# Kernel tuning notes

Hardware: AMD Instinct MI355X
Metric: run time of the kernel (lower is better)

The kernel has to match this reference:

```python
import jax, jax.numpy as jnp
import numpy as np

C = 64          # channels / d_model
D_INNER = 128   # expand * C
D_STATE = 16
D_CONV = 4
DT_RANK = 4     # ceil(C / 16)
GROUPS = 4
EPS = 1e-5


def setup_inputs() -> dict:
    key = jax.random.key(0)
    ks = jax.random.split(key, 12)
    b, h, w = 2, 128, 128
    s = 0.02
    return {
        "x": jax.random.normal(ks[0], (b, C, h, w), jnp.float32),
        "in_proj_w": jax.random.normal(ks[1], (2 * D_INNER, C), jnp.float32) * s,
        "conv_w": jax.random.normal(ks[2], (D_INNER, D_CONV), jnp.float32) * s,
        "conv_b": jnp.zeros((D_INNER,), jnp.float32),
        "x_proj_w": jax.random.normal(ks[3], (DT_RANK + 2 * D_STATE, D_INNER), jnp.float32) * s,
        "dt_proj_w": jax.random.normal(ks[4], (D_INNER, DT_RANK), jnp.float32) * s,
        "dt_proj_b": jax.random.normal(ks[5], (D_INNER,), jnp.float32) * s,
        "A_log": jnp.log(jnp.broadcast_to(jnp.arange(1, D_STATE + 1, dtype=jnp.float32), (D_INNER, D_STATE))),
        "D": jnp.ones((D_INNER,), jnp.float32),
        "out_proj_w": jax.random.normal(ks[6], (C, D_INNER), jnp.float32) * s,
        "gn_scale": jnp.ones((C,), jnp.float32),
        "gn_bias": jnp.zeros((C,), jnp.float32),
    }


def _mamba(xr, in_proj_w, conv_w, conv_b, x_proj_w, dt_proj_w, dt_proj_b, A_log, D, out_proj_w):
    # xr: (b, L, C)
    b, L, _ = xr.shape
    xz = jnp.einsum('blc,ec->ble', xr, in_proj_w)          # (b, L, 2*d_inner)
    xc, z = jnp.split(xz, 2, axis=-1)
    # causal depthwise conv1d, kernel D_CONV
    xp = jnp.pad(xc, ((0, 0), (D_CONV - 1, 0), (0, 0)))
    xconv = sum(conv_w[:, k] * xp[:, k:k + L, :] for k in range(D_CONV)) + conv_b
    u = jax.nn.silu(xconv)                                  # (b, L, d_inner)
    dbc = jnp.einsum('bld,ed->ble', u, x_proj_w)
    dt_r = dbc[..., :DT_RANK]
    Bm = dbc[..., DT_RANK:DT_RANK + D_STATE]                # (b, L, d_state)
    Cm = dbc[..., DT_RANK + D_STATE:]                       # (b, L, d_state)
    dt = jax.nn.softplus(jnp.einsum('blr,dr->bld', dt_r, dt_proj_w) + dt_proj_b)
    A = -jnp.exp(A_log)                                     # (d_inner, d_state)
    deltaA = jnp.exp(dt[..., None] * A)                     # (b, L, d_inner, d_state)
    deltaBu = (dt * u)[..., None] * Bm[:, :, None, :]       # (b, L, d_inner, d_state)

    def step(hst, inp):
        dA_t, dBu_t, C_t = inp
        hst = dA_t * hst + dBu_t                            # (b, d_inner, d_state)
        y_t = jnp.einsum('bds,bs->bd', hst, C_t)
        return hst, y_t

    h0 = jnp.zeros((b, D_INNER, D_STATE), xr.dtype)
    _, ys = jax.lax.scan(step, h0, (jnp.moveaxis(deltaA, 1, 0), jnp.moveaxis(deltaBu, 1, 0), jnp.moveaxis(Cm, 1, 0)))
    y = jnp.moveaxis(ys, 0, 1) + u * D                      # (b, L, d_inner)
    y = y * jax.nn.silu(z)
    return jnp.einsum('bld,cd->blc', y, out_proj_w)


def _group_norm_silu(x, scale, bias):
    # x: (b, C, h, w)
    b, c, h, w = x.shape
    xg = x.reshape(b, GROUPS, c // GROUPS, h, w)
    mu = xg.mean(axis=(2, 3, 4), keepdims=True)
    var = xg.var(axis=(2, 3, 4), keepdims=True)
    xn = ((xg - mu) * jax.lax.rsqrt(var + EPS)).reshape(b, c, h, w)
    return jax.nn.silu(xn * scale[None, :, None, None] + bias[None, :, None, None])


def reference(x, in_proj_w, conv_w, conv_b, x_proj_w, dt_proj_w, dt_proj_b, A_log, D, out_proj_w, gn_scale, gn_bias):
    b, c, h, w = x.shape
    xr = jnp.transpose(x, (0, 2, 3, 1)).reshape(b, h * w, c)
    y = _mamba(xr, in_proj_w, conv_w, conv_b, x_proj_w, dt_proj_w, dt_proj_b, A_log, D, out_proj_w)
    y = jnp.transpose(y.reshape(b, h, w, c), (0, 3, 1, 2))
    y = _group_norm_silu(y, gn_scale, gn_bias)
    return y + x
```

## Files before the change

### kernel.cpp

```cpp
#include <hip/hip_runtime.h>

#define BB 2
#define CCH 64
#define LLEN 16384
#define DM 128
#define NCHK 512
#define TCHK 32
#define NGRP 32
#define JG 16
#define NG 4

#define OFF_XC   0ull
#define OFF_HEND 0ull
#define OFF_HLOC 2097152ull
#define OFF_Z    4194304ull
#define OFF_U    8388608ull
#define OFF_DT   12582912ull
#define OFF_BM   16777216ull
#define OFF_CM   17301504ull
#define OFF_DTS  17825792ull
#define OFF_YM   17956864ull
#define OFF_WC   17956864ull
#define OFF_STAT 20054016ull
#define OFF_CUMDT 20971520ull
#define OFF_GEND  21102592ull
#define OFF_GDT   21233664ull
#define OFF_GINIT 21241856ull

__device__ __forceinline__ float fsilu(float v) {
  return v * __builtin_amdgcn_rcpf(1.f + __expf(-v));
}
__device__ __forceinline__ float fsoftplus(float v) {
  return v > 20.f ? v : __logf(1.f + __expf(v));
}
__device__ __forceinline__ unsigned short f2bf(float f) {
  unsigned u = __builtin_bit_cast(unsigned, f);
  u += 0x7fffu + ((u >> 16) & 1u);
  return (unsigned short)(u >> 16);
}
__device__ __forceinline__ float bf2f(unsigned short h) {
  unsigned u = (unsigned)h << 16;
  return __builtin_bit_cast(float, u);
}

__global__ __launch_bounds__(256) void k0_wcomb(
    const float* __restrict__ xpw, const float* __restrict__ dtw, float* __restrict__ wc,
    float* __restrict__ stat)
{
  int i = blockIdx.x * 256 + threadIdx.x;
  if (blockIdx.x == 0 && threadIdx.x < BB * NG * 2) stat[threadIdx.x] = 0.f;
  if (i >= 160 * 128) return;
  int e = i >> 7, dd = i & 127;
  float v;
  if (e < 128) {
    v = dtw[e * 4 + 0] * xpw[0 * 128 + dd] + dtw[e * 4 + 1] * xpw[1 * 128 + dd]
      + dtw[e * 4 + 2] * xpw[2 * 128 + dd] + dtw[e * 4 + 3] * xpw[3 * 128 + dd];
  } else {
    v = xpw[(e - 128 + 4) * 128 + dd];
  }
  wc[i] = v;
}

__global__ __launch_bounds__(256) void k1_inproj(
    const float* __restrict__ x, const float* __restrict__ w,
    float* __restrict__ xc, float* __restrict__ z)
{
  const int b = blockIdx.z;
  const int l0 = blockIdx.x * 64;
  const int e0 = blockIdx.y * 64;
  __shared__ float As[64][68];
  __shared__ float Bs[64][68];
  const int t = threadIdx.x;
#pragma unroll
  for (int i = 0; i < 4; i++) {
    int f4 = t + i * 256;
    int c = f4 >> 4, tok4 = (f4 & 15) * 4;
    *reinterpret_cast<float4*>(&As[c][tok4]) =
        *reinterpret_cast<const float4*>(&x[(size_t)(b * CCH + c) * LLEN + l0 + tok4]);
  }
#pragma unroll
  for (int i = 0; i < 16; i++) {
    int idx = t + i * 256;
    int e = idx >> 6, c = idx & 63;
    Bs[c][e] = w[(e0 + e) * CCH + c];
  }
  __syncthreads();
  const int tm = (t & 15) * 4;
  const int tn = (t >> 4) * 4;
  float acc[4][4] = {};
  for (int c = 0; c < 64; c++) {
    float4 av = *reinterpret_cast<const float4*>(&As[c][tm]);
    float4 bv = *reinterpret_cast<const float4*>(&Bs[c][tn]);
    acc[0][0] += av.x * bv.x; acc[0][1] += av.x * bv.y; acc[0][2] += av.x * bv.z; acc[0][3] += av.x * bv.w;
    acc[1][0] += av.y * bv.x; acc[1][1] += av.y * bv.y; acc[1][2] += av.y * bv.z; acc[1][3] += av.y * bv.w;
    acc[2][0] += av.z * bv.x; acc[2][1] += av.z * bv.y; acc[2][2] += av.z * bv.z; acc[2][3] += av.z * bv.w;
    acc[3][0] += av.w * bv.x; acc[3][1] += av.w * bv.y; acc[3][2] += av.w * bv.z; acc[3][3] += av.w * bv.w;
  }
  float* dst = (e0 < DM) ? (xc + e0) : (z + (e0 - DM));
#pragma unroll
  for (int i = 0; i < 4; i++) {
    int l = l0 + tm + i;
    float4 v = make_float4(acc[i][0], acc[i][1], acc[i][2], acc[i][3]);
    *reinterpret_cast<float4*>(dst + (size_t)(b * LLEN + l) * DM + tn) = v;
  }
}

__global__ __launch_bounds__(256) void k2a_conv(
    const float* __restrict__ xc, const float* __restrict__ cw, const float* __restrict__ cb,
    float* __restrict__ u)
{
  const int t = threadIdx.x;
  const int d4 = (t & 31) * 4;
  const int tg = t >> 5;
  const int tok0 = blockIdx.x * 64 + tg * 8;
  const int l0 = tok0 & (LLEN - 1);
  float4 w0 = *reinterpret_cast<const float4*>(cw + (d4 + 0) * 4);
  float4 w1 = *reinterpret_cast<const float4*>(cw + (d4 + 1) * 4);
  float4 w2 = *reinterpret_cast<const float4*>(cw + (d4 + 2) * 4);
  float4 w3 = *reinterpret_cast<const float4*>(cw + (d4 + 3) * 4);
  float4 bias = *reinterpret_cast<const float4*>(cb + d4);
  float4 row[11];
#pragma unroll
  for (int r = 0; r < 11; r++) {
    int l = l0 - 3 + r;
    if (l < 0) row[r] = make_float4(0.f, 0.f, 0.f, 0.f);
    else row[r] = *reinterpret_cast<const float4*>(xc + (size_t)(tok0 - 3 + r) * DM + d4);
  }
#pragma unroll
  for (int j = 0; j < 8; j++) {
    float4 acc;
    acc.x = bias.x + w0.x * row[j].x + w0.y * row[j+1].x + w0.z * row[j+2].x + w0.w * row[j+3].x;
    acc.y = bias.y + w1.x * row[j].y + w1.y * row[j+1].y + w1.z * row[j+2].y + w1.w * row[j+3].y;
    acc.z = bias.z + w2.x * row[j].z + w2.y * row[j+1].z + w2.z * row[j+2].z + w2.w * row[j+3].z;
    acc.w = bias.w + w3.x * row[j].w + w3.y * row[j+1].w + w3.z * row[j+2].w + w3.w * row[j+3].w;
    acc.x = fsilu(acc.x); acc.y = fsilu(acc.y); acc.z = fsilu(acc.z); acc.w = fsilu(acc.w);
    *reinterpret_cast<float4*>(u + (size_t)(tok0 + j) * DM + d4) = acc;
  }
}

__global__ __launch_bounds__(128) void k2b_proj(
    const float* __restrict__ u, const float* __restrict__ wc, const float* __restrict__ dtpb,
    float* __restrict__ dt, float* __restrict__ bm, float* __restrict__ cm)
{
  const int tok0 = blockIdx.x * 64;
  const int e0 = blockIdx.y * 32;
  const int t = threadIdx.x;
  __shared__ float As[64][68];
  __shared__ float Bs[64][36];
  const int tm = (t & 15) * 4;
  const int tn = (t >> 4) * 4;
  float acc[4][4] = {};
  for (int kb = 0; kb < 2; kb++) {
#pragma unroll
    for (int i2 = 0; i2 < 2; i2++) {
      int tile = t + i2 * 128;
      int kt4 = (tile & 15) * 4, tok4 = (tile >> 4) * 4;
      const float* gp = u + (size_t)(tok0 + tok4) * DM + kb * 64 + kt4;
      float4 r0 = *reinterpret_cast<const float4*>(gp + 0 * DM);
      float4 r1 = *reinterpret_cast<const float4*>(gp + 1 * DM);
      float4 r2 = *reinterpret_cast<const float4*>(gp + 2 * DM);
      float4 r3 = *reinterpret_cast<const float4*>(gp + 3 * DM);
      *reinterpret_cast<float4*>(&As[kt4 + 0][tok4]) = make_float4(r0.x, r1.x, r2.x, r3.x);
      *reinterpret_cast<float4*>(&As[kt4 + 1][tok4]) = make_float4(r0.y, r1.y, r2.y, r3.y);
      *reinterpret_cast<float4*>(&As[kt4 + 2][tok4]) = make_float4(r0.z, r1.z, r2.z, r3.z);
      *reinterpret_cast<float4*>(&As[kt4 + 3][tok4]) = make_float4(r0.w, r1.w, r2.w, r3.w);
    }
    {
      int kt4 = (t & 15) * 4, et4 = (t >> 4) * 4;
      const float* gp = wc + (size_t)(e0 + et4) * DM + kb * 64 + kt4;
      float4 r0 = *reinterpret_cast<const float4*>(gp + 0 * DM);
      float4 r1 = *reinterpret_cast<const float4*>(gp + 1 * DM);
      float4 r2 = *reinterpret_cast<const float4*>(gp + 2 * DM);
      float4 r3 = *reinterpret_cast<const float4*>(gp + 3 * DM);
      *reinterpret_cast<float4*>(&Bs[kt4 + 0][et4]) = make_float4(r0.x, r1.x, r2.x, r3.x);
      *reinterpret_cast<float4*>(&Bs[kt4 + 1][et4]) = make_float4(r0.y, r1.y, r2.y, r3.y);
      *reinterpret_cast<float4*>(&Bs[kt4 + 2][et4]) = make_float4(r0.z, r1.z, r2.z, r3.z);
      *reinterpret_cast<float4*>(&Bs[kt4 + 3][et4]) = make_float4(r0.w, r1.w, r2.w, r3.w);
    }
    __syncthreads();
#pragma unroll 4
    for (int k = 0; k < 64; k++) {
      float4 av = *reinterpret_cast<const float4*>(&As[k][tm]);
      float4 bv = *reinterpret_cast<const float4*>(&Bs[k][tn]);
      acc[0][0] += av.x * bv.x; acc[0][1] += av.x * bv.y; acc[0][2] += av.x * bv.z; acc[0][3] += av.x * bv.w;
      acc[1][0] += av.y * bv.x; acc[1][1] += av.y * bv.y; acc[1][2] += av.y * bv.z; acc[1][3] += av.y * bv.w;
      acc[2][0] += av.z * bv.x; acc[2][1] += av.z * bv.y; acc[2][2] += av.z * bv.z; acc[2][3] += av.z * bv.w;
      acc[3][0] += av.w * bv.x; acc[3][1] += av.w * bv.y; acc[3][2] += av.w * bv.z; acc[3][3] += av.w * bv.w;
    }
    __syncthreads();
  }
  float* Cs = &As[0][0];
#pragma unroll
  for (int i = 0; i < 4; i++) {
#pragma unroll
    for (int j = 0; j < 4; j++) Cs[(tm + i) * 33 + tn + j] = acc[i][j];
  }
  __syncthreads();
  if (e0 < DM) {
#pragma unroll
    for (int i = 0; i < 16; i++) {
      int idx = t + i * 128;
      int tok = idx >> 5, e = idx & 31;
      float v = fsoftplus(Cs[tok * 33 + e] + dtpb[e0 + e]);
      dt[(size_t)(tok0 + tok) * DM + e0 + e] = v;
    }
  } else {
#pragma unroll
    for (int i = 0; i < 16; i++) {
      int idx = t + i * 128;
      int tok = idx >> 5, e = idx & 31;
      float v = Cs[tok * 33 + e];
      if (e < 16) bm[(size_t)(tok0 + tok) * 16 + e] = v;
      else        cm[(size_t)(tok0 + tok) * 16 + (e - 16)] = v;
    }
  }
}

__global__ __launch_bounds__(128) void k3_scan1(
    const float* __restrict__ dt, const float* __restrict__ u, const float* __restrict__ bm,
    const float* __restrict__ alog, float* __restrict__ hend, float* __restrict__ dts)
{
  const int b = blockIdx.y, ch = blockIdx.x;
  const int d = threadIdx.x;
  __shared__ float sb[TCHK][16];
  const size_t tok0 = (size_t)b * LLEN + (size_t)ch * TCHK;
  reinterpret_cast<float4*>(&sb[0][0])[d] = reinterpret_cast<const float4*>(bm + tok0 * 16)[d];
  float A[16];
  {
    const float4* ap = reinterpret_cast<const float4*>(alog + d * 16);
#pragma unroll
    for (int q = 0; q < 4; q++) {
      float4 v = ap[q];
      A[q * 4 + 0] = -__expf(v.x); A[q * 4 + 1] = -__expf(v.y);
      A[q * 4 + 2] = -__expf(v.z); A[q * 4 + 3] = -__expf(v.w);
    }
  }
  __syncthreads();
  float h[16];
#pragma unroll
  for (int s = 0; s < 16; s++) h[s] = 0.f;
  float dsum = 0.f;
  const float* dtp = dt + tok0 * DM + d;
  const float* up  = u  + tok0 * DM + d;
  for (int i = 0; i < TCHK; i++) {
    float dtv = dtp[(size_t)i * DM];
    float uv  = up[(size_t)i * DM];
    float dtu = dtv * uv;
    dsum += dtv;
    float bv[16];
#pragma unroll
    for (int q = 0; q < 4; q++)
      *reinterpret_cast<float4*>(&bv[q * 4]) = *reinterpret_cast<const float4*>(&sb[i][q * 4]);
#pragma unroll
    for (int s = 0; s < 16; s++) {
      float da = __expf(dtv * A[s]);
      h[s] = da * h[s] + dtu * bv[s];
    }
  }
  float* hp = hend + ((size_t)(b * DM + d) * NCHK + ch) * 16;
#pragma unroll
  for (int q = 0; q < 4; q++)
    reinterpret_cast<float4*>(hp)[q] = make_float4(h[q*4], h[q*4+1], h[q*4+2], h[q*4+3]);
  dts[(size_t)(b * DM + d) * NCHK + ch] = dsum;
}

__global__ __launch_bounds__(256) void k4a_group(
    const float* __restrict__ alog, const float* __restrict__ dts, const float* __restrict__ hend,
    float* __restrict__ hlocal, float* __restrict__ cumdt,
    float* __restrict__ gend, float* __restrict__ gdt)
{
  const int tid = blockIdx.x * 256 + threadIdx.x;
  const int s = tid & 15;
  const int bdg = tid >> 4;
  const int g = bdg & (NGRP - 1);
  const int bd = bdg >> 5;
  const int d = bd & (DM - 1);
  const float A = -__expf(alog[d * 16 + s]);
  const int ch0 = g * JG;
  const float* hp = hend + ((size_t)bd * NCHK + ch0) * 16 + s;
  const float* dp = dts + (size_t)bd * NCHK + ch0;
  float* hl = hlocal + ((size_t)bd * NCHK + ch0) * 16 + s;
  float hb[JG], db[JG];
#pragma unroll
  for (int j = 0; j < JG; j++) { hb[j] = hp[j * 16]; db[j] = dp[j]; }
  float h = 0.f, cd = 0.f;
#pragma unroll
  for (int j = 0; j < JG; j++) {
    hl[j * 16] = h;
    if (s == 0) cumdt[(size_t)(ch0 + j) * (BB * DM) + bd] = cd;
    h = __expf(A * db[j]) * h + hb[j];
    cd += db[j];
  }
  gend[(size_t)bdg * 16 + s] = h;
  if (s == 0) gdt[bdg] = cd;
}

__global__ __launch_bounds__(64) void k4b_combine(
    const float* __restrict__ alog, const float* __restrict__ gdt, const float* __restrict__ gend,
    float* __restrict__ ginit)
{
  const int tid = blockIdx.x * 64 + threadIdx.x;
  const int s = tid & 15, bd = tid >> 4, d = bd & (DM - 1);
  const float A = -__expf(alog[d * 16 + s]);
  const float* ge = gend + (size_t)bd * NGRP * 16 + s;
  const float* gd = gdt + (size_t)bd * NGRP;
  float* gi = ginit + (size_t)bd * NGRP * 16 + s;
  float gb[NGRP], db[NGRP];
#pragma unroll
  for (int g = 0; g < NGRP; g++) { gb[g] = ge[g * 16]; db[g] = gd[g]; }
  float h = 0.f;
#pragma unroll
  for (int g = 0; g < NGRP; g++) {
    gi[g * 16] = h;
    h = __expf(A * db[g]) * h + gb[g];
  }
}

__global__ __launch_bounds__(256) void k5f_scan_out(
    const float* __restrict__ dt, const float* __restrict__ u, const float* __restrict__ bm,
    const float* __restrict__ cm, const float* __restrict__ alog, const float* __restrict__ Dv,
    const float* __restrict__ z, const float* __restrict__ hlocal,
    const float* __restrict__ cumdt, const float* __restrict__ ginit,
    const float* __restrict__ ow, float* __restrict__ ym, float* __restrict__ stat)
{
  const int b = blockIdx.y, bx = blockIdx.x;
  const int t = threadIdx.x;
  const int ch2 = t >> 7;
  const int d = t & 127;
  const int ch = bx * 2 + ch2;
  __shared__ float sb[2][TCHK][16];
  __shared__ float sc[2][TCHK][16];
  __shared__ unsigned short Ysb[DM][72];
  __shared__ unsigned short Bsb[DM][68];
  const size_t tokb = (size_t)b * LLEN + (size_t)bx * 64;
  const size_t tok0 = tokb + (size_t)ch2 * TCHK;
  reinterpret_cast<float4*>(&sb[0][0][0])[t] = reinterpret_cast<const float4*>(bm + tokb * 16)[t];
  reinterpret_cast<float4*>(&sc[0][0][0])[t] = reinterpret_cast<const float4*>(cm + tokb * 16)[t];
#pragma unroll
  for (int i2 = 0; i2 < 2; i2++) {
    int tile = t + i2 * 256;
    int c4 = (tile & 15) * 4;
    int dl4 = (tile >> 4) * 4;
    const float* gp = ow + (size_t)c4 * DM + dl4;
    float4 r0 = *reinterpret_cast<const float4*>(gp + 0 * DM);
    float4 r1 = *reinterpret_cast<const float4*>(gp + 1 * DM);
    float4 r2 = *reinterpret_cast<const float4*>(gp + 2 * DM);
    float4 r3 = *reinterpret_cast<const float4*>(gp + 3 * DM);
    ushort4 w0 = make_ushort4(f2bf(r0.x), f2bf(r1.x), f2bf(r2.x), f2bf(r3.x));
    ushort4 w1 = make_ushort4(f2bf(r0.y), f2bf(r1.y), f2bf(r2.y), f2bf(r3.y));
    ushort4 w2 = make_ushort4(f2bf(r0.z), f2bf(r1.z), f2bf(r2.z), f2bf(r3.z));
    ushort4 w3 = make_ushort4(f2bf(r0.w), f2bf(r1.w), f2bf(r2.w), f2bf(r3.w));
    *reinterpret_cast<ushort4*>(&Bsb[dl4 + 0][c4]) = w0;
    *reinterpret_cast<ushort4*>(&Bsb[dl4 + 1][c4]) = w1;
    *reinterpret_cast<ushort4*>(&Bsb[dl4 + 2][c4]) = w2;
    *reinterpret_cast<ushort4*>(&Bsb[dl4 + 3][c4]) = w3;
  }
  float A[16];
  {
    const float4* ap = reinterpret_cast<const float4*>(alog + d * 16);
#pragma unroll
    for (int q = 0; q < 4; q++) {
      float4 v = ap[q];
      A[q * 4 + 0] = -__expf(v.x); A[q * 4 + 1] = -__expf(v.y);
      A[q * 4 + 2] = -__expf(v.z); A[q * 4 + 3] = -__expf(v.w);
    }
  }
  const float Dd = Dv[d];
  const int bd = b * DM + d;
  const int g = ch / JG;
  const float cd = cumdt[(size_t)ch * (BB * DM) + bd];
  float h[16];
  {
    const float4* hlp = reinterpret_cast<const float4*>(hlocal + ((size_t)bd * NCHK + ch) * 16);
    const float4* gip = reinterpret_cast<const float4*>(ginit + ((size_t)(bd * NGRP + g)) * 16);
#pragma unroll
    for (int q = 0; q < 4; q++) {
      float4 hl = hlp[q];
      float4 gi = gip[q];
      h[q * 4 + 0] = __expf(A[q * 4 + 0] * cd) * gi.x + hl.x;
      h[q * 4 + 1] = __expf(A[q * 4 + 1] * cd) * gi.y + hl.y;
      h[q * 4 + 2] = __expf(A[q * 4 + 2] * cd) * gi.z + hl.z;
      h[q * 4 + 3] = __expf(A[q * 4 + 3] * cd) * gi.w + hl.w;
    }
  }
  __syncthreads();
  const float* dtp = dt + tok0 * DM + d;
  const float* up = u + tok0 * DM + d;
  const float* zp = z + tok0 * DM + d;
  for (int i = 0; i < TCHK; i++) {
    float dtv = dtp[(size_t)i * DM];
    float uv  = up[(size_t)i * DM];
    float zv  = zp[(size_t)i * DM];
    float dtu = dtv * uv;
    float bv[16], cv[16];
#pragma unroll
    for (int q = 0; q < 4; q++) {
      *reinterpret_cast<float4*>(&bv[q * 4]) = *reinterpret_cast<const float4*>(&sb[ch2][i][q * 4]);
      *reinterpret_cast<float4*>(&cv[q * 4]) = *reinterpret_cast<const float4*>(&sc[ch2][i][q * 4]);
    }
    float y = 0.f;
#pragma unroll
    for (int s = 0; s < 16; s++) {
      float da = __expf(dtv * A[s]);
      h[s] = da * h[s] + dtu * bv[s];
      y += h[s] * cv[s];
    }
    Ysb[d][ch2 * TCHK + i] = f2bf((y + uv * Dd) * fsilu(zv));
  }
  __syncthreads();
  const int tm = (t & 15) * 4;
  const int tn = (t >> 4) * 4;
  float acc[4][4] = {};
  for (int k = 0; k < DM; k++) {
    ushort4 a4 = *reinterpret_cast<const ushort4*>(&Ysb[k][tm]);
    ushort4 b4 = *reinterpret_cast<const ushort4*>(&Bsb[k][tn]);
    float ax = bf2f(a4.x), ay = bf2f(a4.y), az = bf2f(a4.z), aw = bf2f(a4.w);
    float bx2 = bf2f(b4.x), by = bf2f(b4.y), bz = bf2f(b4.z), bw = bf2f(b4.w);
    acc[0][0] += ax * bx2; acc[0][1] += ax * by; acc[0][2] += ax * bz; acc[0][3] += ax * bw;
    acc[1][0] += ay * bx2; acc[1][1] += ay * by; acc[1][2] += ay * bz; acc[1][3] += ay * bw;
    acc[2][0] += az * bx2; acc[2][1] += az * by; acc[2][2] += az * bz; acc[2][3] += az * bw;
    acc[3][0] += aw * bx2; acc[3][1] += aw * by; acc[3][2] += aw * bz; acc[3][3] += aw * bw;
  }
  float lsum = 0.f, lssq = 0.f;
#pragma unroll
  for (int i = 0; i < 4; i++) {
    float4 v = make_float4(acc[i][0], acc[i][1], acc[i][2], acc[i][3]);
    *reinterpret_cast<float4*>(ym + (tokb + tm + i) * 64 + tn) = v;
    lsum += v.x + v.y + v.z + v.w;
    lssq += v.x * v.x + v.y * v.y + v.z * v.z + v.w * v.w;
  }
  __shared__ float sg[NG * 2];
  if (t < NG * 2) sg[t] = 0.f;
  __syncthreads();
  const int gg = tn >> 4;
  atomicAdd(&sg[gg * 2 + 0], lsum);
  atomicAdd(&sg[gg * 2 + 1], lssq);
  __syncthreads();
  if (t < NG * 2) atomicAdd(&stat[b * NG * 2 + t], sg[t]);
}

__global__ __launch_bounds__(256) void k7_gn(
    const float* __restrict__ ym, const float* __restrict__ stat,
    const float* __restrict__ scale, const float* __restrict__ bias,
    const float* __restrict__ x, float* __restrict__ out)
{
  const int b = blockIdx.y;
  const int p0 = blockIdx.x * 64;
  const int t = threadIdx.x;
  __shared__ float Ts[64][65];
#pragma unroll
  for (int i = 0; i < 16; i++) {
    int idx = t + i * 256;
    int p = idx >> 6, c = idx & 63;
    Ts[c][p] = ym[(size_t)(b * LLEN + p0 + p) * 64 + c];
  }
  __syncthreads();
  const float invN = 1.f / (16.f * 16384.f);
#pragma unroll
  for (int i = 0; i < 16; i++) {
    int idx = t + i * 256;
    int c = idx >> 6, p = idx & 63;
    int g = c >> 4;
    float mu = stat[b * 8 + g * 2] * invN;
    float var = stat[b * 8 + g * 2 + 1] * invN - mu * mu;
    float rs = rsqrtf(var + 1e-5f);
    float v = (Ts[c][p] - mu) * rs * scale[c] + bias[c];
    size_t o = (size_t)(b * CCH + c) * LLEN + p0 + p;
    out[o] = fsilu(v) + x[o];
  }
}

extern "C" void kernel_launch(void* const* d_in, const int* in_sizes, int n_in,
                              void* d_out, int out_size, void* d_ws, size_t ws_size,
                              hipStream_t stream)
{
  const float* x    = (const float*)d_in[0];
  const float* ipw  = (const float*)d_in[1];
  const float* cw   = (const float*)d_in[2];
  const float* cb   = (const float*)d_in[3];
  const float* xpw  = (const float*)d_in[4];
  const float* dtw  = (const float*)d_in[5];
  const float* dtpb = (const float*)d_in[6];
  const float* alog = (const float*)d_in[7];
  const float* Dv   = (const float*)d_in[8];
  const float* ow   = (const float*)d_in[9];
  const float* gns  = (const float*)d_in[10];
  const float* gnb  = (const float*)d_in[11];

  float* ws    = (float*)d_ws;
  float* xc    = ws + OFF_XC;
  float* hend  = ws + OFF_HEND;
  float* hloc  = ws + OFF_HLOC;
  float* z     = ws + OFF_Z;
  float* u     = ws + OFF_U;
  float* dt    = ws + OFF_DT;
  float* bm    = ws + OFF_BM;
  float* cm    = ws + OFF_CM;
  float* dts   = ws + OFF_DTS;
  float* ym    = ws + OFF_YM;
  float* wc    = ws + OFF_WC;
  float* cumdt = ws + OFF_CUMDT;
  float* gend  = ws + OFF_GEND;
  float* gdt   = ws + OFF_GDT;
  float* ginit = ws + OFF_GINIT;
  float* stat  = ws + OFF_STAT;
  float* out   = (float*)d_out;

  k0_wcomb<<<dim3(80), 256, 0, stream>>>(xpw, dtw, wc, stat);
  k1_inproj<<<dim3(LLEN / 64, 4, BB), 256, 0, stream>>>(x, ipw, xc, z);
  k2a_conv<<<dim3(BB * LLEN / 64), 256, 0, stream>>>(xc, cw, cb, u);
  k2b_proj<<<dim3(BB * LLEN / 64, 5), 128, 0, stream>>>(u, wc, dtpb, dt, bm, cm);
  k3_scan1<<<dim3(NCHK, BB), 128, 0, stream>>>(dt, u, bm, alog, hend, dts);
  k4a_group<<<dim3(BB * DM * NGRP * 16 / 256), 256, 0, stream>>>(alog, dts, hend, hloc, cumdt, gend, gdt);
  k4b_combine<<<dim3(BB * DM * 16 / 64), 64, 0, stream>>>(alog, gdt, gend, ginit);
  k5f_scan_out<<<dim3(NCHK / 2, BB), 256, 0, stream>>>(dt, u, bm, cm, alog, Dv, z, hloc, cumdt, ginit, ow, ym, stat);
  k7_gn<<<dim3(LLEN / 64, BB), 256, 0, stream>>>(ym, stat, gns, gnb, x, out);
}
```

Measured before the change: 136.1 us.

## Halve scan chunk length to double parallel chunks and use 512-thread scan-out blocks

After: 141.8 us. 1.04x slower.

```diff
diff --git a/kernel.cpp b/kernel.cpp
--- a/kernel.cpp
+++ b/kernel.cpp
@@ -4,28 +4,28 @@
 #define CCH 64
 #define LLEN 16384
 #define DM 128
-#define NCHK 512
-#define TCHK 32
+#define NCHK 1024
+#define TCHK 16
 #define NGRP 32
-#define JG 16
+#define JG 32
 #define NG 4
 
-#define OFF_XC   0ull
-#define OFF_HEND 0ull
-#define OFF_HLOC 2097152ull
-#define OFF_Z    4194304ull
-#define OFF_U    8388608ull
-#define OFF_DT   12582912ull
-#define OFF_BM   16777216ull
-#define OFF_CM   17301504ull
-#define OFF_DTS  17825792ull
-#define OFF_YM   17956864ull
-#define OFF_WC   17956864ull
-#define OFF_STAT 20054016ull
-#define OFF_CUMDT 20971520ull
-#define OFF_GEND  21102592ull
-#define OFF_GDT   21233664ull
-#define OFF_GINIT 21241856ull
+#define OFF_XC    0ull
+#define OFF_HEND  0ull
+#define OFF_Z     4194304ull
+#define OFF_U     8388608ull
+#define OFF_DT    12582912ull
+#define OFF_BM    16777216ull
+#define OFF_CM    17301504ull
+#define OFF_DTS   17825792ull
+#define OFF_YM    18088192ull
+#define OFF_WC    18088192ull
+#define OFF_STAT  20185344ull
+#define OFF_HLOC  20185600ull
+#define OFF_CUMDT 24379904ull
+#define OFF_GEND  24642048ull
+#define OFF_GDT   24773120ull
+#define OFF_GINIT 24781312ull
 
 __device__ __forceinline__ float fsilu(float v) {
   return v * __builtin_amdgcn_rcpf(1.f + __expf(-v));
@@ -224,7 +224,8 @@
   const int d = threadIdx.x;
   __shared__ float sb[TCHK][16];
   const size_t tok0 = (size_t)b * LLEN + (size_t)ch * TCHK;
-  reinterpret_cast<float4*>(&sb[0][0])[d] = reinterpret_cast<const float4*>(bm + tok0 * 16)[d];
+  if (d < TCHK * 4)
+    reinterpret_cast<float4*>(&sb[0][0])[d] = reinterpret_cast<const float4*>(bm + tok0 * 16)[d];
   float A[16];
   {
     const float4* ap = reinterpret_cast<const float4*>(alog + d * 16);
@@ -316,7 +317,7 @@
   }
 }
 
-__global__ __launch_bounds__(256) void k5f_scan_out(
+__global__ __launch_bounds__(512) void k5f_scan_out(
     const float* __restrict__ dt, const float* __restrict__ u, const float* __restrict__ bm,
     const float* __restrict__ cm, const float* __restrict__ alog, const float* __restrict__ Dv,
     const float* __restrict__ z, const float* __restrict__ hlocal,
@@ -325,22 +326,22 @@
 {
   const int b = blockIdx.y, bx = blockIdx.x;
   const int t = threadIdx.x;
-  const int ch2 = t >> 7;
+  const int ch4 = t >> 7;
   const int d = t & 127;
-  const int ch = bx * 2 + ch2;
-  __shared__ float sb[2][TCHK][16];
-  __shared__ float sc[2][TCHK][16];
+  const int ch = bx * 4 + ch4;
+  __shared__ float sb[4][TCHK][16];
+  __shared__ float sc[4][TCHK][16];
   __shared__ unsigned short Ysb[DM][72];
   __shared__ unsigned short Bsb[DM][68];
   const size_t tokb = (size_t)b * LLEN + (size_t)bx * 64;
-  const size_t tok0 = tokb + (size_t)ch2 * TCHK;
-  reinterpret_cast<float4*>(&sb[0][0][0])[t] = reinterpret_cast<const float4*>(bm + tokb * 16)[t];
-  reinterpret_cast<float4*>(&sc[0][0][0])[t] = reinterpret_cast<const float4*>(cm + tokb * 16)[t];
-#pragma unroll
-  for (int i2 = 0; i2 < 2; i2++) {
-    int tile = t + i2 * 256;
-    int c4 = (tile & 15) * 4;
-    int dl4 = (tile >> 4) * 4;
+  const size_t tok0 = tokb + (size_t)ch4 * TCHK;
+  if (t < 256) {
+    reinterpret_cast<float4*>(&sb[0][0][0])[t] = reinterpret_cast<const float4*>(bm + tokb * 16)[t];
+    reinterpret_cast<float4*>(&sc[0][0][0])[t] = reinterpret_cast<const float4*>(cm + tokb * 16)[t];
+  }
+  {
+    int c4 = (t & 15) * 4;
+    int dl4 = (t >> 4) * 4;
     const float* gp = ow + (size_t)c4 * DM + dl4;
     float4 r0 = *reinterpret_cast<const float4*>(gp + 0 * DM);
     float4 r1 = *reinterpret_cast<const float4*>(gp + 1 * DM);
@@ -395,8 +396,8 @@
     float bv[16], cv[16];
 #pragma unroll
     for (int q = 0; q < 4; q++) {
-      *reinterpret_cast<float4*>(&bv[q * 4]) = *reinterpret_cast<const float4*>(&sb[ch2][i][q * 4]);
-      *reinterpret_cast<float4*>(&cv[q * 4]) = *reinterpret_cast<const float4*>(&sc[ch2][i][q * 4]);
+      *reinterpret_cast<float4*>(&bv[q * 4]) = *reinterpret_cast<const float4*>(&sb[ch4][i][q * 4]);
+      *reinterpret_cast<float4*>(&cv[q * 4]) = *reinterpret_cast<const float4*>(&sc[ch4][i][q * 4]);
     }
     float y = 0.f;
 #pragma unroll
@@ -405,34 +406,32 @@
       h[s] = da * h[s] + dtu * bv[s];
       y += h[s] * cv[s];
     }
-    Ysb[d][ch2 * TCHK + i] = f2bf((y + uv * Dd) * fsilu(zv));
-  }
-  __syncthreads();
-  const int tm = (t & 15) * 4;
-  const int tn = (t >> 4) * 4;
-  float acc[4][4] = {};
+    Ysb[d][ch4 * TCHK + i] = f2bf((y + uv * Dd) * fsilu(zv));
+  }
+  __syncthreads();
+  const int tm2 = (t & 31) * 2;
+  const int tn4 = (t >> 5) * 4;
+  float acc[2][4] = {};
   for (int k = 0; k < DM; k++) {
-    ushort4 a4 = *reinterpret_cast<const ushort4*>(&Ysb[k][tm]);
-    ushort4 b4 = *reinterpret_cast<const ushort4*>(&Bsb[k][tn]);
-    float ax = bf2f(a4.x), ay = bf2f(a4.y), az = bf2f(a4.z), aw = bf2f(a4.w);
+    ushort2 a2 = *reinterpret_cast<const ushort2*>(&Ysb[k][tm2]);
+    ushort4 b4 = *reinterpret_cast<const ushort4*>(&Bsb[k][tn4]);
+    float ax = bf2f(a2.x), ay = bf2f(a2.y);
     float bx2 = bf2f(b4.x), by = bf2f(b4.y), bz = bf2f(b4.z), bw = bf2f(b4.w);
     acc[0][0] += ax * bx2; acc[0][1] += ax * by; acc[0][2] += ax * bz; acc[0][3] += ax * bw;
     acc[1][0] += ay * bx2; acc[1][1] += ay * by; acc[1][2] += ay * bz; acc[1][3] += ay * bw;
-    acc[2][0] += az * bx2; acc[2][1] += az * by; acc[2][2] += az * bz; acc[2][3] += az * bw;
-    acc[3][0] += aw * bx2; acc[3][1] += aw * by; acc[3][2] += aw * bz; acc[3][3] += aw * bw;
   }
   float lsum = 0.f, lssq = 0.f;
 #pragma unroll
-  for (int i = 0; i < 4; i++) {
+  for (int i = 0; i < 2; i++) {
     float4 v = make_float4(acc[i][0], acc[i][1], acc[i][2], acc[i][3]);
-    *reinterpret_cast<float4*>(ym + (tokb + tm + i) * 64 + tn) = v;
+    *reinterpret_cast<float4*>(ym + (tokb + tm2 + i) * 64 + tn4) = v;
     lsum += v.x + v.y + v.z + v.w;
     lssq += v.x * v.x + v.y * v.y + v.z * v.z + v.w * v.w;
   }
   __shared__ float sg[NG * 2];
   if (t < NG * 2) sg[t] = 0.f;
   __syncthreads();
-  const int gg = tn >> 4;
+  const int gg = tn4 >> 4;
   atomicAdd(&sg[gg * 2 + 0], lsum);
   atomicAdd(&sg[gg * 2 + 1], lssq);
   __syncthreads();
@@ -513,6 +512,6 @@
   k3_scan1<<<dim3(NCHK, BB), 128, 0, stream>>>(dt, u, bm, alog, hend, dts);
   k4a_group<<<dim3(BB * DM * NGRP * 16 / 256), 256, 0, stream>>>(alog, dts, hend, hloc, cumdt, gend, gdt);
   k4b_combine<<<dim3(BB * DM * 16 / 64), 64, 0, stream>>>(alog, gdt, gend, ginit);
-  k5f_scan_out<<<dim3(NCHK / 2, BB), 256, 0, stream>>>(dt, u, bm, cm, alog, Dv, z, hloc, cumdt, ginit, ow, ym, stat);
+  k5f_scan_out<<<dim3(NCHK / 4, BB), 512, 0, stream>>>(dt, u, bm, cm, alog, Dv, z, hloc, cumdt, ginit, ow, ym, stat);
   k7_gn<<<dim3(LLEN / 64, BB), 256, 0, stream>>>(ym, stat, gns, gnb, x, out);
 }
```
